# Kernel tuning notes

Hardware: AMD Instinct MI355X
Metric: run time of the kernel (lower is better)

The kernel has to match this reference:

```python
import jax, jax.numpy as jnp
from jax import lax
import numpy as np

B, C, A, K = 8, 64, 9, 90          # batch, BiFPN channels, anchors/cell, classes
NC = 3                              # num conv layers in each subnet (D0)
SIZES = [64, 32, 16, 8, 4]          # P3..P7 spatial sizes for 512x512 input
NL = len(SIZES)
BN_EPS = 1e-3
PRIOR_BIAS = -float(np.log((1.0 - 0.01) / 0.01))  # focal-loss prior init


def setup_inputs() -> dict:
    key = jax.random.key(0)
    ks = iter(jax.random.split(key, 64))
    inp = {}
    for i, s in enumerate(SIZES):
        inp[f"p{i+3}"] = jax.random.normal(next(ks), (B, C, s, s), jnp.float32)
    dw_std = np.float32(np.sqrt(1.0 / (9.0 * C)))   # TF fan_in init, depthwise 3x3
    pw_std = np.float32(np.sqrt(1.0 / C))           # pointwise 1x1
    # shared subnet conv weights (stacked over depth)
    for pre in ("cls", "box"):
        inp[f"{pre}_dw"] = jax.random.normal(next(ks), (NC, C, 1, 3, 3), jnp.float32) * dw_std
        inp[f"{pre}_pw"] = jax.random.normal(next(ks), (NC, C, C), jnp.float32) * pw_std
        inp[f"{pre}_pw_b"] = jnp.zeros((NC, C), jnp.float32)
    # per-level, per-depth BatchNorm params (inference mode: running stats)
    for pre in ("cls", "box"):
        inp[f"bn_{pre}_g"] = jnp.ones((NL, NC, C), jnp.float32) + 0.1 * jax.random.normal(next(ks), (NL, NC, C), jnp.float32)
        inp[f"bn_{pre}_b"] = 0.1 * jax.random.normal(next(ks), (NL, NC, C), jnp.float32)
        inp[f"bn_{pre}_m"] = 0.1 * jax.random.normal(next(ks), (NL, NC, C), jnp.float32)
        inp[f"bn_{pre}_v"] = jax.random.uniform(next(ks), (NL, NC, C), jnp.float32, 0.5, 1.5)
    # output heads
    inp["score_dw"] = jax.random.normal(next(ks), (C, 1, 3, 3), jnp.float32) * dw_std
    inp["score_pw"] = jax.random.normal(next(ks), (A * K, C), jnp.float32) * pw_std
    inp["score_b"] = jnp.full((A * K,), PRIOR_BIAS, jnp.float32)
    inp["pred_dw"] = jax.random.normal(next(ks), (C, 1, 3, 3), jnp.float32) * dw_std
    inp["pred_pw"] = jax.random.normal(next(ks), (A * 4, C), jnp.float32) * pw_std
    inp["pred_b"] = jnp.zeros((A * 4,), jnp.float32)
    return inp


def _sep_conv(x, dw, pw, b):
    """SeparableConvBlock: depthwise 3x3 (SAME) + pointwise 1x1 with bias."""
    y = lax.conv_general_dilated(
        x, dw, window_strides=(1, 1), padding="SAME",
        dimension_numbers=("NCHW", "OIHW", "NCHW"), feature_group_count=x.shape[1])
    y = jnp.einsum("nchw,oc->nohw", y, pw)
    return y + b[None, :, None, None]


def _bn(x, g, b, m, v):
    scale = (g / jnp.sqrt(v + BN_EPS))[None, :, None, None]
    return (x - m[None, :, None, None]) * scale + b[None, :, None, None]


def _swish(x):
    return x * jax.nn.sigmoid(x)


def reference(p3, p4, p5, p6, p7,
              cls_dw, cls_pw, cls_pw_b, box_dw, box_pw, box_pw_b,
              bn_cls_g, bn_cls_b, bn_cls_m, bn_cls_v,
              bn_box_g, bn_box_b, bn_box_m, bn_box_v,
              score_dw, score_pw, score_b, pred_dw, pred_pw, pred_b):
    feats = [p3, p4, p5, p6, p7]
    logits, bbox_reg = [], []
    for lvl, f in enumerate(feats):
        xc, xb = f, f
        for d in range(NC):  # shared conv weights across levels, per-level BN
            xc = _swish(_bn(_sep_conv(xc, cls_dw[d], cls_pw[d], cls_pw_b[d]),
                            bn_cls_g[lvl, d], bn_cls_b[lvl, d], bn_cls_m[lvl, d], bn_cls_v[lvl, d]))
            xb = _swish(_bn(_sep_conv(xb, box_dw[d], box_pw[d], box_pw_b[d]),
                            bn_box_g[lvl, d], bn_box_b[lvl, d], bn_box_m[lvl, d], bn_box_v[lvl, d]))
        logits.append(_sep_conv(xc, score_dw, score_pw, score_b))      # (N, A*K, H, W)
        bbox_reg.append(_sep_conv(xb, pred_dw, pred_pw, pred_b))       # (N, A*4, H, W)
    return tuple(logits) + tuple(bbox_reg)
```

## Files before the change

### kernel.cpp

```cpp
#include <hip/hip_runtime.h>


namespace {
constexpr int CH = 64;
constexpr int NCD = 3;
constexpr long S = 2793472;
constexpr int TPI = 86;
constexpr int TPS = 688;
constexpr int TOT = 43648;
constexpr float BNEPS = 1e-3f;
constexpr int WSTR_S = 896;
constexpr int NCHUNK = 171;
constexpr int GEMM_BLOCKS = NCHUNK * 9;
constexpr int QXC = GEMM_BLOCKS / 8;
constexpr int RXC = GEMM_BLOCKS - 8 * QXC;
}

__device__ __forceinline__ int wave_id() {
  return __builtin_amdgcn_readfirstlane((int)(threadIdx.x >> 6));
}

__device__ __forceinline__ void decode_tile(int u, int& lvl, int& tx0, int& ty0) {
  int tile, tpr;
  if (u < 64)       { lvl = 0; tile = u;      tpr = 8; }
  else if (u < 80)  { lvl = 1; tile = u - 64; tpr = 4; }
  else if (u < 84)  { lvl = 2; tile = u - 80; tpr = 2; }
  else if (u == 84) { lvl = 3; tile = 0;      tpr = 1; }
  else              { lvl = 4; tile = 0;      tpr = 1; }
  tx0 = (tile % tpr) * 8;
  ty0 = (tile / tpr) * 8;
}

__device__ __forceinline__ long lvl_off(int lvl) {
  switch (lvl) {
    case 0: return 0L;
    case 1: return 2097152L;
    case 2: return 2621440L;
    case 3: return 2752512L;
    default: return 2785280L;
  }
}

__device__ __forceinline__ int lvl_lb(int lvl) {
  switch (lvl) {
    case 0: return 0;
    case 1: return 32768;
    case 2: return 40960;
    case 3: return 43008;
    default: return 43520;
  }
}

__device__ __forceinline__ long head_out_base(int subnet, int lvl) {
  if (subnet == 0) {
    switch (lvl) {
      case 0: return 0L;
      case 1: return 26542080L;
      case 2: return 33177600L;
      case 3: return 34836480L;
      default: return 35251200L;
    }
  } else {
    switch (lvl) {
      case 0: return 35354880L;
      case 1: return 36534528L;
      case 2: return 36829440L;
      case 3: return 36903168L;
      default: return 36921600L;
    }
  }
}

__global__ __launch_bounds__(256) void prep_stage_kernel(
    const float* __restrict__ cls_pw, const float* __restrict__ box_pw,
    float* __restrict__ wcT) {
  int i = blockIdx.x * 256 + threadIdx.x;
  if (i >= 2 * NCD * CH * CH) return;
  int o = i & 63;
  int c = (i >> 6) & 63;
  int sd = i >> 12;
  const float* src = (sd < NCD) ? cls_pw : box_pw;
  int d = (sd < NCD) ? sd : sd - NCD;
  wcT[i] = src[(d * CH + o) * CH + c];
}

__global__ __launch_bounds__(256) void prep_head_kernel(
    const float* __restrict__ score_pw, const float* __restrict__ pred_pw,
    float* __restrict__ wT, float* __restrict__ wpT) {
  int i = blockIdx.x * 256 + threadIdx.x;
  if (i < CH * WSTR_S) {
    int c = i / WSTR_S;
    int o = i - c * WSTR_S;
    wT[i] = (o < 810) ? score_pw[o * CH + c] : 0.f;
  } else {
    int j = i - CH * WSTR_S;
    if (j < CH * CH) {
      int c = j >> 6;
      int o = j & 63;
      wpT[j] = (o < 36) ? pred_pw[o * CH + c] : 0.f;
    }
  }
}

__global__ __launch_bounds__(256) void stage_kernel(
    const float* __restrict__ q0, const float* __restrict__ q1,
    const float* __restrict__ q2, const float* __restrict__ q3,
    const float* __restrict__ q4,
    const float* __restrict__ buf_in, float* __restrict__ buf_out,
    const float* __restrict__ cls_dw, const float* __restrict__ box_dw,
    const float* __restrict__ wcT,
    const float* __restrict__ cls_pwb, const float* __restrict__ box_pwb,
    const float* __restrict__ bng0, const float* __restrict__ bnb0,
    const float* __restrict__ bnm0, const float* __restrict__ bnv0,
    const float* __restrict__ bng1, const float* __restrict__ bnb1,
    const float* __restrict__ bnm1, const float* __restrict__ bnv1,
    int depth)
{
  __shared__ float s_in[CH * 120];

  int bx = blockIdx.x;
  int subnet = bx / TPS;
  int r = bx - subnet * TPS;
  int n = r / TPI;
  int u = r - n * TPI;
  int lvl, tx0, ty0;
  decode_tile(u, lvl, tx0, ty0);
  int H = 64 >> lvl;

  const float* in;
  if (depth == 0) {
    in = (lvl == 0) ? q0 : (lvl == 1) ? q1 : (lvl == 2) ? q2 : (lvl == 3) ? q3 : q4;
  } else {
    in = buf_in + (long)subnet * S + lvl_off(lvl);
  }
  const float* dww = subnet ? box_dw : cls_dw;
  const float* pwb = subnet ? box_pwb : cls_pwb;
  const float* bg = subnet ? bng1 : bng0;
  const float* bb = subnet ? bnb1 : bnb0;
  const float* bm = subnet ? bnm1 : bnm0;
  const float* bv = subnet ? bnv1 : bnv0;

  int t = threadIdx.x;
  long img_base = (long)n * CH * H * H;

  for (int idx = t; idx < CH * 100; idx += 256) {
    int c = idx / 100;
    int rem = idx - c * 100;
    int yy = rem / 10;
    int xx = rem - yy * 10;
    int gy = ty0 - 1 + yy, gx = tx0 - 1 + xx;
    float v = 0.f;
    if (gy >= 0 && gy < H && gx >= 0 && gx < H)
      v = in[img_base + ((long)c * H + gy) * H + gx];
    s_in[c * 120 + yy * 12 + xx] = v;
  }
  __syncthreads();

  int px = t & 63;
  int pxx = px & 7, pxy = px >> 3;
  int w = wave_id();

  #pragma unroll
  for (int k = 0; k < 16; ++k) {
    int c = w + 4 * k;
    const float* dwc = dww + ((long)depth * CH + c) * 9;
    const float* base = &s_in[c * 120 + pxy * 12 + pxx];
    float a = 0.f;
    #pragma unroll
    for (int dy = 0; dy < 3; ++dy)
      #pragma unroll
      for (int dx = 0; dx < 3; ++dx)
        a = fmaf(dwc[dy * 3 + dx], base[dy * 12 + dx], a);
    s_in[c * 120 + pxy * 12 + pxx] = a;
  }
  __syncthreads();

  const float* wc = wcT + ((subnet * NCD + depth) * CH) * CH + w * 16;
  float acc[16];
  #pragma unroll
  for (int k = 0; k < 16; ++k) acc[k] = 0.f;
  #pragma unroll 4
  for (int c = 0; c < CH; ++c) {
    float v = s_in[c * 120 + pxy * 12 + pxx];
    const float* wr = wc + c * CH;
    #pragma unroll
    for (int k = 0; k < 16; ++k)
      acc[k] = fmaf(wr[k], v, acc[k]);
  }

  int ox = tx0 + pxx, oy = ty0 + pxy;
  if (ox < H && oy < H) {
    float* outp = buf_out + (long)subnet * S + lvl_off(lvl) + img_base;
    int bno = (lvl * NCD + depth) * CH;
    #pragma unroll
    for (int k = 0; k < 16; ++k) {
      int o = w * 16 + k;
      float scale = bg[bno + o] * rsqrtf(bv[bno + o] + BNEPS);
      float z = fmaf(acc[k] + pwb[depth * CH + o] - bm[bno + o], scale, bb[bno + o]);
      float y = z / (1.f + __expf(-z));
      outp[((long)o * H + oy) * H + ox] = y;
    }
  }
}

__global__ __launch_bounds__(256) void head_dw_kernel(
    const float* __restrict__ buf_in, float* __restrict__ dv,
    const float* __restrict__ score_dw, const float* __restrict__ pred_dw)
{
  __shared__ float s_in[CH * 120];

  int bx = blockIdx.x;
  int subnet = bx / TPS;
  int r = bx - subnet * TPS;
  int n = r / TPI;
  int u = r - n * TPI;
  int lvl, tx0, ty0;
  decode_tile(u, lvl, tx0, ty0);
  int H = 64 >> lvl;

  const float* in = buf_in + (long)subnet * S + lvl_off(lvl);
  const float* dww = subnet ? pred_dw : score_dw;
  float* dvs = dv + (long)subnet * S;

  int t = threadIdx.x;
  long img_base = (long)n * CH * H * H;

  for (int idx = t; idx < CH * 100; idx += 256) {
    int c = idx / 100;
    int rem = idx - c * 100;
    int yy = rem / 10;
    int xx = rem - yy * 10;
    int gy = ty0 - 1 + yy, gx = tx0 - 1 + xx;
    float v = 0.f;
    if (gy >= 0 && gy < H && gx >= 0 && gx < H)
      v = in[img_base + ((long)c * H + gy) * H + gx];
    s_in[c * 120 + yy * 12 + xx] = v;
  }
  __syncthreads();

  int px = t & 63;
  int pxx = px & 7, pxy = px >> 3;
  int w = wave_id();

  int ox = tx0 + pxx, oy = ty0 + pxy;
  bool valid = (ox < H) && (oy < H);
  int fp = lvl_lb(lvl) + n * H * H + oy * H + ox;

  #pragma unroll
  for (int k = 0; k < 16; ++k) {
    int c = w + 4 * k;
    const float* dwc = dww + c * 9;
    const float* base = &s_in[c * 120 + pxy * 12 + pxx];
    float a = 0.f;
    #pragma unroll
    for (int dy = 0; dy < 3; ++dy)
      #pragma unroll
      for (int dx = 0; dx < 3; ++dx)
        a = fmaf(dwc[dy * 3 + dx], base[dy * 12 + dx], a);
    if (valid) dvs[c * TOT + fp] = a;
  }
}

__global__ __launch_bounds__(256, 4) void head_gemm_kernel(
    const float* __restrict__ dv, const float* __restrict__ wT,
    const float* __restrict__ wpT,
    const float* __restrict__ score_b, const float* __restrict__ pred_b,
    float* __restrict__ out)
{
  int lane = threadIdx.x & 63;
  int wid = wave_id();

  int b = blockIdx.x;
  int xk = b & 7, xi = b >> 3;
  int job = (xk < RXC) ? xk * (QXC + 1) + xi
                       : RXC * (QXC + 1) + (xk - RXC) * QXC + xi;
  int pxc = job / 9;
  int sub = job - pxc * 9;

  int fp0 = pxc * 256 + wid * 64;
  if (fp0 >= TOT) return;

  int subnet = (sub == 8) ? 1 : 0;

  int lvl, lb, lsh;
  if (fp0 < 32768)      { lvl = 0; lb = 0;     lsh = 12; }
  else if (fp0 < 40960) { lvl = 1; lb = 32768; lsh = 10; }
  else if (fp0 < 43008) { lvl = 2; lb = 40960; lsh = 8;  }
  else if (fp0 < 43520) { lvl = 3; lb = 43008; lsh = 6;  }
  else                  { lvl = 4; lb = 43520; lsh = 4;  }
  int HH = 1 << lsh;

  int OC = subnet ? 36 : 810;
  int wstr = subnet ? CH : WSTR_S;
  const float* wtab = subnet ? wpT : wT;
  const float* btab = subnet ? pred_b : score_b;

  const float* dvp = dv + (long)subnet * S + fp0 + lane;
  float dvr[64];
  #pragma unroll
  for (int c = 0; c < CH; ++c) dvr[c] = dvp[c * TOT];

  int rem = fp0 + lane - lb;
  int n = rem >> lsh;
  int r2 = rem & (HH - 1);
  long pbase = head_out_base(subnet, lvl) + (long)n * OC * HH + r2;

  int o_begin = subnet ? 0 : sub * 112;
  int o_end = subnet ? 48 : (sub * 112 + 112 < 832 ? sub * 112 + 112 : 832);

  for (int o0 = o_begin; o0 < o_end; o0 += 16) {
    const float* wp = wtab + o0;
    float acc[16];
    #pragma unroll
    for (int k = 0; k < 16; ++k) acc[k] = 0.f;
    #pragma unroll 8
    for (int c = 0; c < CH; ++c) {
      const float* wr = wp + c * wstr;
      float v = dvr[c];
      #pragma unroll
      for (int k = 0; k < 16; ++k)
        acc[k] = fmaf(wr[k], v, acc[k]);
    }
    #pragma unroll
    for (int k = 0; k < 16; ++k) {
      int o = o0 + k;
      if (o < OC)
        out[pbase + (long)o * HH] = acc[k] + btab[o];
    }
  }
}

extern "C" void kernel_launch(void* const* d_in, const int* in_sizes, int n_in,
                              void* d_out, int out_size, void* d_ws, size_t ws_size,
                              hipStream_t stream) {
  const float* p3 = (const float*)d_in[0];
  const float* p4 = (const float*)d_in[1];
  const float* p5 = (const float*)d_in[2];
  const float* p6 = (const float*)d_in[3];
  const float* p7 = (const float*)d_in[4];
  const float* cls_dw = (const float*)d_in[5];
  const float* cls_pw = (const float*)d_in[6];
  const float* cls_pwb = (const float*)d_in[7];
  const float* box_dw = (const float*)d_in[8];
  const float* box_pw = (const float*)d_in[9];
  const float* box_pwb = (const float*)d_in[10];
  const float* bn_cls_g = (const float*)d_in[11];
  const float* bn_cls_b = (const float*)d_in[12];
  const float* bn_cls_m = (const float*)d_in[13];
  const float* bn_cls_v = (const float*)d_in[14];
  const float* bn_box_g = (const float*)d_in[15];
  const float* bn_box_b = (const float*)d_in[16];
  const float* bn_box_m = (const float*)d_in[17];
  const float* bn_box_v = (const float*)d_in[18];
  const float* score_dw = (const float*)d_in[19];
  const float* score_pw = (const float*)d_in[20];
  const float* score_b = (const float*)d_in[21];
  const float* pred_dw = (const float*)d_in[22];
  const float* pred_pw = (const float*)d_in[23];
  const float* pred_b = (const float*)d_in[24];

  float* ws = (float*)d_ws;
  float* out = (float*)d_out;
  float* buf0 = ws;
  float* buf1 = ws + 2 * S;
  float* dv = buf1;
  float* wcT = out;
  float* wT = ws;
  float* wpT = ws + CH * WSTR_S;

  dim3 blk(256);
  prep_stage_kernel<<<dim3(96), blk, 0, stream>>>(cls_pw, box_pw, wcT);
  stage_kernel<<<dim3(2 * TPS), blk, 0, stream>>>(
      p3, p4, p5, p6, p7, nullptr, buf0, cls_dw, box_dw, wcT, cls_pwb, box_pwb,
      bn_cls_g, bn_cls_b, bn_cls_m, bn_cls_v,
      bn_box_g, bn_box_b, bn_box_m, bn_box_v, 0);
  stage_kernel<<<dim3(2 * TPS), blk, 0, stream>>>(
      p3, p4, p5, p6, p7, buf0, buf1, cls_dw, box_dw, wcT, cls_pwb, box_pwb,
      bn_cls_g, bn_cls_b, bn_cls_m, bn_cls_v,
      bn_box_g, bn_box_b, bn_box_m, bn_box_v, 1);
  stage_kernel<<<dim3(2 * TPS), blk, 0, stream>>>(
      p3, p4, p5, p6, p7, buf1, buf0, cls_dw, box_dw, wcT, cls_pwb, box_pwb,
      bn_cls_g, bn_cls_b, bn_cls_m, bn_cls_v,
      bn_box_g, bn_box_b, bn_box_m, bn_box_v, 2);
  head_dw_kernel<<<dim3(2 * TPS), blk, 0, stream>>>(buf0, dv, score_dw, pred_dw);
  prep_head_kernel<<<dim3(240), blk, 0, stream>>>(score_pw, pred_pw, wT, wpT);
  head_gemm_kernel<<<dim3(GEMM_BLOCKS), blk, 0, stream>>>(
      dv, wT, wpT, score_b, pred_b, out);
}
```

Baseline: 497.5 us.

## Stage head GEMM activations in LDS and split output channels across waves

```diff
diff --git a/kernel.cpp b/kernel.cpp
--- a/kernel.cpp
+++ b/kernel.cpp
@@ -10,8 +10,8 @@
 constexpr int TOT = 43648;
 constexpr float BNEPS = 1e-3f;
 constexpr int WSTR_S = 896;
-constexpr int NCHUNK = 171;
-constexpr int GEMM_BLOCKS = NCHUNK * 9;
+constexpr int NSB = 14;
+constexpr int GEMM_BLOCKS = 682 * NSB;
 constexpr int QXC = GEMM_BLOCKS / 8;
 constexpr int RXC = GEMM_BLOCKS - 8 * QXC;
 }
@@ -261,26 +261,40 @@
   }
 }
 
-__global__ __launch_bounds__(256, 4) void head_gemm_kernel(
+__global__ __launch_bounds__(256) void head_gemm_kernel(
     const float* __restrict__ dv, const float* __restrict__ wT,
     const float* __restrict__ wpT,
     const float* __restrict__ score_b, const float* __restrict__ pred_b,
     float* __restrict__ out)
 {
-  int lane = threadIdx.x & 63;
+  __shared__ float s_dv[CH * 64];
+
+  int b = blockIdx.x;
+  int xcd = b & 7, xi = b >> 3;
+  int job = (xcd < RXC) ? xcd * (QXC + 1) + xi
+                        : RXC * (QXC + 1) + (xcd - RXC) * QXC + xi;
+  int pxt = job / NSB;
+  int sb = job - pxt * NSB;
+  int subnet = (sb == NSB - 1) ? 1 : 0;
+
+  int fp0 = pxt * 64;
+  int t = threadIdx.x;
+
+  const float* dvs = dv + (long)subnet * S + fp0;
+  for (int idx = t; idx < CH * 64; idx += 256) {
+    int c = idx >> 6;
+    int px = idx & 63;
+    s_dv[idx] = dvs[(long)c * TOT + px];
+  }
+  __syncthreads();
+
+  int lane = t & 63;
   int wid = wave_id();
 
-  int b = blockIdx.x;
-  int xk = b & 7, xi = b >> 3;
-  int job = (xk < RXC) ? xk * (QXC + 1) + xi
-                       : RXC * (QXC + 1) + (xk - RXC) * QXC + xi;
-  int pxc = job / 9;
-  int sub = job - pxc * 9;
-
-  int fp0 = pxc * 256 + wid * 64;
-  if (fp0 >= TOT) return;
-
-  int subnet = (sub == 8) ? 1 : 0;
+  int st;
+  if (subnet == 0) { st = sb * 4 + wid; if (st >= 51) return; }
+  else             { st = wid;          if (st >= 3)  return; }
+  int o0 = st * 16;
 
   int lvl, lb, lsh;
   if (fp0 < 32768)      { lvl = 0; lb = 0;     lsh = 12; }
@@ -295,38 +309,29 @@
   const float* wtab = subnet ? wpT : wT;
   const float* btab = subnet ? pred_b : score_b;
 
-  const float* dvp = dv + (long)subnet * S + fp0 + lane;
-  float dvr[64];
-  #pragma unroll
-  for (int c = 0; c < CH; ++c) dvr[c] = dvp[c * TOT];
+  float acc[16];
+  #pragma unroll
+  for (int k = 0; k < 16; ++k) acc[k] = 0.f;
+  const float* wp = wtab + o0;
+  #pragma unroll 8
+  for (int c = 0; c < CH; ++c) {
+    float v = s_dv[c * 64 + lane];
+    const float* wr = wp + c * wstr;
+    #pragma unroll
+    for (int k = 0; k < 16; ++k)
+      acc[k] = fmaf(wr[k], v, acc[k]);
+  }
 
   int rem = fp0 + lane - lb;
   int n = rem >> lsh;
   int r2 = rem & (HH - 1);
   long pbase = head_out_base(subnet, lvl) + (long)n * OC * HH + r2;
 
-  int o_begin = subnet ? 0 : sub * 112;
-  int o_end = subnet ? 48 : (sub * 112 + 112 < 832 ? sub * 112 + 112 : 832);
-
-  for (int o0 = o_begin; o0 < o_end; o0 += 16) {
-    const float* wp = wtab + o0;
-    float acc[16];
-    #pragma unroll
-    for (int k = 0; k < 16; ++k) acc[k] = 0.f;
-    #pragma unroll 8
-    for (int c = 0; c < CH; ++c) {
-      const float* wr = wp + c * wstr;
-      float v = dvr[c];
-      #pragma unroll
-      for (int k = 0; k < 16; ++k)
-        acc[k] = fmaf(wr[k], v, acc[k]);
-    }
-    #pragma unroll
-    for (int k = 0; k < 16; ++k) {
-      int o = o0 + k;
-      if (o < OC)
-        out[pbase + (long)o * HH] = acc[k] + btab[o];
-    }
+  #pragma unroll
+  for (int k = 0; k < 16; ++k) {
+    int o = o0 + k;
+    if (o < OC)
+      out[pbase + (long)o * HH] = acc[k] + btab[o];
   }
 }
 
```

Measured after the change: 430.5 us. -13.5%, faster.
